# Performance work log

Measured on AMD Instinct MI355X. Metric: run time of the kernel, lower is better.

## Reference

```python
import jax, jax.numpy as jnp
import numpy as np

N_NODES = 100000
N_EDGES = 1600000
EMBED = 64
HEADS = 8
HEAD_DIM = EMBED // HEADS
FFN = 4 * EMBED
EPS = 1e-5


def _layer_norm(x, g, b):
    m = jnp.mean(x, axis=-1, keepdims=True)
    v = jnp.mean(jnp.square(x - m), axis=-1, keepdims=True)
    return (x - m) * jax.lax.rsqrt(v + EPS) * g + b


def setup_inputs() -> dict:
    key = jax.random.key(0)
    ks = jax.random.split(key, 10)
    s = lambda fan_in: 1.0 / np.sqrt(fan_in)
    x = jax.random.normal(ks[0], (N_NODES, EMBED), dtype=jnp.float32)
    edge_indices = jax.random.randint(ks[1], (2, N_EDGES), 0, N_NODES, dtype=jnp.int64)
    attn_w = jax.random.uniform(ks[2], (EMBED, 3 * EMBED), jnp.float32, -s(EMBED), s(EMBED))
    attn_b = jnp.zeros((3 * EMBED,), jnp.float32)
    w1 = jax.random.uniform(ks[3], (EMBED, FFN), jnp.float32, -s(EMBED), s(EMBED))
    b1 = jnp.zeros((FFN,), jnp.float32)
    w2 = jax.random.uniform(ks[4], (FFN, EMBED), jnp.float32, -s(FFN), s(FFN))
    b2 = jnp.zeros((EMBED,), jnp.float32)
    ln1_g = jnp.ones((EMBED,), jnp.float32)
    ln1_b = jnp.zeros((EMBED,), jnp.float32)
    ln2_g = jnp.ones((EMBED,), jnp.float32)
    ln2_b = jnp.zeros((EMBED,), jnp.float32)
    return {"x": x, "edge_indices": edge_indices, "attn_w": attn_w, "attn_b": attn_b,
            "w1": w1, "b1": b1, "w2": w2, "b2": b2,
            "ln1_g": ln1_g, "ln1_b": ln1_b, "ln2_g": ln2_g, "ln2_b": ln2_b}


def _self_attention(x, edge_indices, attn_w, attn_b):
    n = x.shape[0]
    row, col = edge_indices[0], edge_indices[1]
    scale = EMBED ** (-0.5)  # note: original scales by embed_dim**-0.5
    qkv = (x @ attn_w + attn_b).reshape(n, HEADS, 3 * HEAD_DIM)
    q, k, v = jnp.split(qkv, 3, axis=2)  # each [N, H, Dh]
    alpha = jnp.sum(q[row] * k[col], axis=2) * scale  # [E, H]
    # sparse per-row softmax via segment reductions
    m = jax.ops.segment_max(alpha, row, num_segments=n)  # [N, H]
    e = jnp.exp(alpha - m[row])
    denom = jax.ops.segment_sum(e, row, num_segments=n)  # [N, H]
    weights = e / denom[row]  # [E, H]
    vals = v[col] * weights[:, :, None]  # [E, H, Dh]
    out = jax.ops.segment_sum(vals, row, num_segments=n)  # [N, H, Dh]
    return out.reshape(n, EMBED)


def reference(x, edge_indices, attn_w, attn_b, w1, b1, w2, b2, ln1_g, ln1_b, ln2_g, ln2_b):
    # post-norm (norm_first=False), dropout=0
    x = _layer_norm(x + _self_attention(x, edge_indices, attn_w, attn_b), ln1_g, ln1_b)
    ffn = jax.nn.relu(x @ w1 + b1) @ w2 + b2
    x = _layer_norm(x + ffn, ln2_g, ln2_b)
    return x
```

## Files before the change

### kernel.cpp

```cpp
#include <hip/hip_runtime.h>
#include <hip/hip_bf16.h>
#include <hip/hip_fp8.h>


#define WAVE 64
constexpr int BUCKET_SHIFT = 7;
constexpr int NBMAX = 800;

typedef __attribute__((ext_vector_type(8))) short bf16x8;
typedef __attribute__((ext_vector_type(4))) float f32x4;
typedef __attribute__((ext_vector_type(2))) float f32x2;

__device__ __forceinline__ float bfbits_lo(unsigned u) {
  return __uint_as_float(u << 16);
}
__device__ __forceinline__ float bfbits_hi(unsigned u) {
  return __uint_as_float(u & 0xffff0000u);
}
__device__ __forceinline__ unsigned f2bf_pk(float a, float b) {
  unsigned ua = __float_as_uint(a);
  unsigned ub = __float_as_uint(b);
  ua = (ua + 0x7fff + ((ua >> 16) & 1)) >> 16;
  ub = (ub + 0x7fff + ((ub >> 16) & 1)) & 0xffff0000u;
  return ua | ub;
}
__device__ __forceinline__ unsigned short f2bf1(float a) {
  unsigned ua = __float_as_uint(a);
  ua = (ua + 0x7fff + ((ua >> 16) & 1)) >> 16;
  return (unsigned short)ua;
}

#if defined(__has_builtin)
#if __has_builtin(__builtin_amdgcn_cvt_pk_f32_fp8) && \
    __has_builtin(__builtin_amdgcn_cvt_pk_fp8_f32)
#define FP8_HW 1
#endif
#endif

#ifdef FP8_HW
#define FP8PK0(w) __builtin_amdgcn_cvt_pk_f32_fp8((int)(w), false)
#define FP8PK1(w) __builtin_amdgcn_cvt_pk_f32_fp8((int)(w), true)
__device__ __forceinline__ unsigned fp8enc4(float a, float b, float c,
                                            float d) {
  int r = __builtin_amdgcn_cvt_pk_fp8_f32(a, b, 0, false);
  r = __builtin_amdgcn_cvt_pk_fp8_f32(c, d, r, true);
  return (unsigned)r;
}
#else
__device__ __forceinline__ f32x2 fp8pk_sw(unsigned w, int sh) {
  __hip_fp8_e4m3 a, b;
  a.__x = (unsigned char)((w >> sh) & 0xff);
  b.__x = (unsigned char)((w >> (sh + 8)) & 0xff);
  f32x2 r;
  r.x = (float)a;
  r.y = (float)b;
  return r;
}
#define FP8PK0(w) fp8pk_sw((w), 0)
#define FP8PK1(w) fp8pk_sw((w), 16)
__device__ __forceinline__ unsigned fp8enc4(float a, float b, float c,
                                            float d) {
  __hip_fp8_e4m3 qa(a), qb(b), qc(c), qd(d);
  return (unsigned)qa.__x | ((unsigned)qb.__x << 8) |
         ((unsigned)qc.__x << 16) | ((unsigned)qd.__x << 24);
}
#endif

__device__ __forceinline__ float dot8_fp8(uint2 w, const float qv[8]) {
  f32x2 a = FP8PK0(w.x), b = FP8PK1(w.x), c = FP8PK0(w.y), d = FP8PK1(w.y);
  return a.x * qv[0] + a.y * qv[1] + b.x * qv[2] + b.y * qv[3] + c.x * qv[4] +
         c.y * qv[5] + d.x * qv[6] + d.y * qv[7];
}
__device__ __forceinline__ void acc8_fp8(uint2 w, float ee, float acc[8]) {
  f32x2 a = FP8PK0(w.x), b = FP8PK1(w.x), c = FP8PK0(w.y), d = FP8PK1(w.y);
  acc[0] += ee * a.x;
  acc[1] += ee * a.y;
  acc[2] += ee * b.x;
  acc[3] += ee * b.y;
  acc[4] += ee * c.x;
  acc[5] += ee * c.y;
  acc[6] += ee * d.x;
  acc[7] += ee * d.y;
}

__global__ __launch_bounds__(256) void cvt_w2(
    const float* __restrict__ aw, const float* __restrict__ w1,
    const float* __restrict__ w2, unsigned short* __restrict__ awT,
    unsigned short* __restrict__ w1T, unsigned short* __restrict__ w2T) {
  int tid = blockIdx.x * 256 + threadIdx.x;
  int stride = gridDim.x * 256;
  for (int i = tid; i < 192 * 64; i += stride) {
    int nn = i >> 6, kk = i & 63;
    awT[i] = f2bf1(aw[kk * 192 + nn]);
  }
  for (int i = tid; i < 256 * 64; i += stride) {
    int nn = i >> 6, kk = i & 63;
    w1T[i] = f2bf1(w1[kk * 256 + nn]);
  }
  for (int i = tid; i < 64 * 256; i += stride) {
    int nn = i >> 8, kk = i & 255;
    w2T[i] = f2bf1(w2[kk * 64 + nn]);
  }
}

__global__ __launch_bounds__(256) void cvt_x(const float* __restrict__ x,
                                             unsigned short* __restrict__ xb,
                                             int total8) {
  int i = blockIdx.x * 256 + threadIdx.x;
  int stride = gridDim.x * 256;
  const float4* xf = (const float4*)x;
  uint4* xo = (uint4*)xb;
  for (; i < total8; i += stride) {
    float4 a = xf[2 * i], b = xf[2 * i + 1];
    uint4 st = make_uint4(f2bf_pk(a.x, a.y), f2bf_pk(a.z, a.w),
                          f2bf_pk(b.x, b.y), f2bf_pk(b.z, b.w));
    xo[i] = st;
  }
}

template <int NCOLS, int K, int MODE>
__global__ __launch_bounds__(256) void mfma_gemm(
    const unsigned short* __restrict__ A, const unsigned short* __restrict__ BT,
    const float* __restrict__ bias, unsigned short* __restrict__ out_q,
    unsigned char* __restrict__ out_kv8, unsigned short* __restrict__ out_h,
    const unsigned short* __restrict__ resid, const float* __restrict__ g,
    const float* __restrict__ beta, float* __restrict__ out_f, int n) {
  constexpr int KP = K + 8;
  constexpr int NT = NCOLS / 16;
  constexpr int NKC = K / 32;
  __shared__ unsigned short sB[NCOLS * KP];

  const int tid = threadIdx.x;
  {
    const uint4* src = (const uint4*)BT;
    for (int idx = tid; idx < NCOLS * K / 8; idx += 256) {
      int nn = idx / (K / 8), kq = idx % (K / 8);
      *(uint4*)&sB[nn * KP + kq * 8] = src[idx];
    }
  }
  __syncthreads();

  const int wid = tid >> 6, lane = tid & 63;
  const int l15 = lane & 15, quad = lane >> 4;
  const int rowbase = blockIdx.x * 128 + wid * 32;

  bf16x8 afrag[2][NKC];
#pragma unroll
  for (int rg = 0; rg < 2; rg++) {
    int row = rowbase + rg * 16 + l15;
    if (row >= n) row = n - 1;
    const bf16x8* ap = (const bf16x8*)(A + (size_t)row * K);
#pragma unroll
    for (int kc = 0; kc < NKC; kc++) afrag[rg][kc] = ap[kc * 4 + quad];
  }

  f32x4 acc[2][NT];
#pragma unroll
  for (int rg = 0; rg < 2; rg++)
#pragma unroll
    for (int t = 0; t < NT; t++) acc[rg][t] = (f32x4){0.f, 0.f, 0.f, 0.f};

#pragma unroll
  for (int t = 0; t < NT; t++) {
#pragma unroll
    for (int kc = 0; kc < NKC; kc++) {
      bf16x8 b = *(const bf16x8*)&sB[(t * 16 + l15) * KP + kc * 32 + quad * 8];
      acc[0][t] = __builtin_amdgcn_mfma_f32_16x16x32_bf16(b, afrag[0][kc],
                                                          acc[0][t], 0, 0, 0);
      acc[1][t] = __builtin_amdgcn_mfma_f32_16x16x32_bf16(b, afrag[1][kc],
                                                          acc[1][t], 0, 0, 0);
    }
  }

  if (MODE == 0) {
#pragma unroll
    for (int rg = 0; rg < 2; rg++) {
      int row = rowbase + rg * 16 + l15;
      if (row >= n) continue;
#pragma unroll
      for (int t = 0; t < NT; t++) {
        int c0 = t * 16 + quad * 4;
        float4 bb = *(const float4*)&bias[c0];
        float v0 = acc[rg][t].x + bb.x, v1 = acc[rg][t].y + bb.y;
        float v2 = acc[rg][t].z + bb.z, v3 = acc[rg][t].w + bb.w;
        int hh = c0 / 24, rem = c0 % 24;
        if (rem < 8) {
          v0 *= 0.125f;
          v1 *= 0.125f;
          v2 *= 0.125f;
          v3 *= 0.125f;
          *(uint2*)(out_q + (size_t)row * 64 + hh * 8 + rem) =
              make_uint2(f2bf_pk(v0, v1), f2bf_pk(v2, v3));
        } else if (rem < 16) {
          *(unsigned*)(out_kv8 + (size_t)row * 128 + hh * 8 + (rem - 8)) =
              fp8enc4(v0, v1, v2, v3);
        } else {
          *(unsigned*)(out_kv8 + (size_t)row * 128 + 64 + hh * 8 + (rem - 16)) =
              fp8enc4(v0, v1, v2, v3);
        }
      }
    }
  } else if (MODE == 1) {
#pragma unroll
    for (int rg = 0; rg < 2; rg++) {
      int row = rowbase + rg * 16 + l15;
      if (row >= n) continue;
#pragma unroll
      for (int t = 0; t < NT; t++) {
        int c0 = t * 16 + quad * 4;
        float4 bb = *(const float4*)&bias[c0];
        float v0 = fmaxf(acc[rg][t].x + bb.x, 0.f);
        float v1 = fmaxf(acc[rg][t].y + bb.y, 0.f);
        float v2 = fmaxf(acc[rg][t].z + bb.z, 0.f);
        float v3 = fmaxf(acc[rg][t].w + bb.w, 0.f);
        *(uint2*)(out_h + (size_t)row * NCOLS + c0) =
            make_uint2(f2bf_pk(v0, v1), f2bf_pk(v2, v3));
      }
    }
  } else {
#pragma unroll
    for (int rg = 0; rg < 2; rg++) {
      int row = rowbase + rg * 16 + l15;
      bool ok = row < n;
      int rowc = ok ? row : n - 1;
      float vals[4][4];
      float ps = 0.f, pq = 0.f;
#pragma unroll
      for (int t = 0; t < 4; t++) {
        int c0 = t * 16 + quad * 4;
        float4 bb = *(const float4*)&bias[c0];
        uint2 rr = *(const uint2*)&resid[(size_t)rowc * 64 + c0];
        vals[t][0] = acc[rg][t].x + bb.x + bfbits_lo(rr.x);
        vals[t][1] = acc[rg][t].y + bb.y + bfbits_hi(rr.x);
        vals[t][2] = acc[rg][t].z + bb.z + bfbits_lo(rr.y);
        vals[t][3] = acc[rg][t].w + bb.w + bfbits_hi(rr.y);
#pragma unroll
        for (int r = 0; r < 4; r++) {
          ps += vals[t][r];
          pq += vals[t][r] * vals[t][r];
        }
      }
      ps += __shfl_xor(ps, 16);
      ps += __shfl_xor(ps, 32);
      pq += __shfl_xor(pq, 16);
      pq += __shfl_xor(pq, 32);
      float mean = ps * (1.f / 64.f);
      float var = pq * (1.f / 64.f) - mean * mean;
      float inv = rsqrtf(var + 1e-5f);
      if (ok) {
#pragma unroll
        for (int t = 0; t < 4; t++) {
          int c0 = t * 16 + quad * 4;
          float4 gg = *(const float4*)&g[c0];
          float4 be = *(const float4*)&beta[c0];
          float4 o = make_float4((vals[t][0] - mean) * inv * gg.x + be.x,
                                 (vals[t][1] - mean) * inv * gg.y + be.y,
                                 (vals[t][2] - mean) * inv * gg.z + be.z,
                                 (vals[t][3] - mean) * inv * gg.w + be.w);
          *(float4*)&out_f[(size_t)row * 64 + c0] = o;
        }
      }
    }
  }
}

__global__ void detect_kernel(const int* __restrict__ e, unsigned* flag) {
  unsigned v = 0;
  for (int i = threadIdx.x; i < 2048; i += 256) v |= (unsigned)e[2 * i + 1];
#pragma unroll
  for (int m = 1; m < WAVE; m <<= 1) v |= (unsigned)__shfl_xor((int)v, m);
  if ((threadIdx.x & 63) == 0 && v) atomicOr(flag, 1u);
}

__device__ __forceinline__ int edge_row(const int* e, int i, bool is64) {
  return is64 ? e[2 * (size_t)i] : e[i];
}
__device__ __forceinline__ int edge_col(const int* e, int i, int E, bool is64) {
  return is64 ? e[2 * ((size_t)E + i)] : e[(size_t)E + i];
}

__global__ __launch_bounds__(256) void partition_count(
    const int* __restrict__ e, int E, const unsigned* __restrict__ flag,
    int* __restrict__ G, int NB, int CH) {
  __shared__ int h[NBMAX];
  bool is64 = (*flag == 0u);
  for (int b = threadIdx.x; b < NB; b += 256) h[b] = 0;
  __syncthreads();
  int c0 = blockIdx.x * CH, c1 = min(E, c0 + CH);
  for (int i = c0 + threadIdx.x; i < c1; i += 256)
    atomicAdd(&h[edge_row(e, i, is64) >> BUCKET_SHIFT], 1);
  __syncthreads();
  for (int b = threadIdx.x; b < NB; b += 256) G[b * 256 + blockIdx.x] = h[b];
}

__global__ __launch_bounds__(1024) void scan_reduce(const int* __restrict__ in,
                                                    int n,
                                                    int* __restrict__ bsum) {
  __shared__ int sdata[16];
  int tid = threadIdx.x;
  int idx = blockIdx.x * 1024 + tid;
  int v = (idx < n) ? in[idx] : 0;
#pragma unroll
  for (int m = 1; m < WAVE; m <<= 1) v += __shfl_xor(v, m);
  if ((tid & 63) == 0) sdata[tid >> 6] = v;
  __syncthreads();
  if (tid < 16) {
    int s = sdata[tid];
#pragma unroll
    for (int m = 1; m < 16; m <<= 1) s += __shfl_xor(s, m);
    if (tid == 0) bsum[blockIdx.x] = s;
  }
}

__global__ __launch_bounds__(256) void scan_top(const int* __restrict__ bsum,
                                                int nb, int* __restrict__ bpre) {
  __shared__ int wsum[4];
  int tid = threadIdx.x;
  int lane = tid & 63, wid = tid >> 6;
  int v = (tid < nb) ? bsum[tid] : 0;
  int incl = v;
#pragma unroll
  for (int m = 1; m < WAVE; m <<= 1) {
    int t = __shfl_up(incl, m);
    if (lane >= m) incl += t;
  }
  if (lane == 63) wsum[wid] = incl;
  __syncthreads();
  int add = 0;
  for (int w = 0; w < wid; w++) add += wsum[w];
  if (tid < nb) bpre[tid] = add + incl - v;
}

__global__ __launch_bounds__(1024) void scan_apply(
    const int* __restrict__ in, int n, const int* __restrict__ bpre,
    int* __restrict__ outscan) {
  __shared__ int wtot[16];
  __shared__ int wexcl[16];
  int tid = threadIdx.x;
  int idx = blockIdx.x * 1024 + tid;
  int v = (idx < n) ? in[idx] : 0;
  int incl = v;
#pragma unroll
  for (int m = 1; m < WAVE; m <<= 1) {
    int t = __shfl_up(incl, m);
    if ((tid & 63) >= m) incl += t;
  }
  int wid = tid >> 6;
  if ((tid & 63) == 63) wtot[wid] = incl;
  __syncthreads();
  if (tid < 16) {
    int w = wtot[tid];
    int wi = w;
#pragma unroll
    for (int m = 1; m < 16; m <<= 1) {
      int t = __shfl_up(wi, m);
      if (tid >= m) wi += t;
    }
    wexcl[tid] = wi - w;
  }
  __syncthreads();
  if (idx < n) outscan[idx] = bpre[blockIdx.x] + wexcl[wid] + incl - v;
}

__global__ __launch_bounds__(256) void partition_scatter(
    const int* __restrict__ e, int E, const unsigned* __restrict__ flag,
    const int* __restrict__ scanG, unsigned* __restrict__ ebuf, int NB,
    int CH) {
  __shared__ int base[NBMAX];
  bool is64 = (*flag == 0u);
  for (int b = threadIdx.x; b < NB; b += 256)
    base[b] = scanG[b * 256 + blockIdx.x];
  __syncthreads();
  int c0 = blockIdx.x * CH, c1 = min(E, c0 + CH);
  for (int i = c0 + threadIdx.x; i < c1; i += 256) {
    int r = edge_row(e, i, is64);
    int c = edge_col(e, i, E, is64);
    int pos = atomicAdd(&base[r >> BUCKET_SHIFT], 1);
    ebuf[pos] = ((unsigned)(r & 127) << 17) | (unsigned)c;
  }
}

__global__ __launch_bounds__(256) void bucket_csr(
    const unsigned* __restrict__ ebuf, const int* __restrict__ scanG,
    int* __restrict__ ecol, int* __restrict__ rowstart, int n, int NB, int E) {
  __shared__ int cnt[128], offs[128], cur[128];
  const int b = blockIdx.x;
  const int tid = threadIdx.x;
  const int start = scanG[b * 256];
  const int end = (b + 1 < NB) ? scanG[(b + 1) * 256] : E;
  if (tid < 128) cnt[tid] = 0;
  __syncthreads();
  for (int i = start + tid; i < end; i += 256)
    atomicAdd(&cnt[(ebuf[i] >> 17) & 127], 1);
  __syncthreads();
  if (tid < 128) offs[tid] = cnt[tid];
  __syncthreads();
  for (int s = 1; s < 128; s <<= 1) {
    int t = 0;
    if (tid < 128 && tid >= s) t = offs[tid - s];
    __syncthreads();
    if (tid < 128) offs[tid] += t;
    __syncthreads();
  }
  if (tid < 128) {
    int excl = offs[tid] - cnt[tid];
    cur[tid] = start + excl;
    int gr = (b << BUCKET_SHIFT) + tid;
    if (gr < n) rowstart[gr] = start + excl;
  }
  if (b == NB - 1 && tid == 0) rowstart[n] = E;
  __syncthreads();
  for (int i = start + tid; i < end; i += 256) {
    unsigned p = ebuf[i];
    int pos = atomicAdd(&cur[(p >> 17) & 127], 1);
    ecol[pos] = (int)(p & 0x1FFFF);
  }
}

__global__ __launch_bounds__(256) void attn_ln_kernel(
    const unsigned short* __restrict__ xb,
    const unsigned short* __restrict__ qbuf,
    const unsigned char* __restrict__ kv8, const int* __restrict__ rowstart,
    const int* __restrict__ ecol, const float* __restrict__ g,
    const float* __restrict__ beta, unsigned short* __restrict__ x1b, int n) {
  int wave = threadIdx.x >> 6;
  int lane = threadIdx.x & 63;
  int node = blockIdx.x * 4 + wave;
  if (node >= n) return;
  const int e = lane >> 3, h = lane & 7;

  uint4 qp = ((const uint4*)(qbuf + (size_t)node * 64))[h];
  float qv[8] = {bfbits_lo(qp.x), bfbits_hi(qp.x), bfbits_lo(qp.y),
                 bfbits_hi(qp.y), bfbits_lo(qp.z), bfbits_hi(qp.z),
                 bfbits_lo(qp.w), bfbits_hi(qp.w)};

  int start = rowstart[node];
  int cnt = rowstart[node + 1] - start;
  float den = 0.f;
  float acc[8] = {0.f, 0.f, 0.f, 0.f, 0.f, 0.f, 0.f, 0.f};

  int iters = (cnt + 7) >> 3;
  int it = 0;
  for (; it + 2 <= iters; it += 2) {
    int i0 = it * 8 + e;
    int i1 = i0 + 8;
    bool v1 = i1 < cnt;
    int c0 = ecol[start + i0];
    int c1 = ecol[start + (v1 ? i1 : i0)];
    const unsigned char* r0 = kv8 + (size_t)c0 * 128 + h * 8;
    const unsigned char* r1 = kv8 + (size_t)c1 * 128 + h * 8;
    uint2 kw0 = *(const uint2*)r0;
    uint2 vw0 = *(const uint2*)(r0 + 64);
    uint2 kw1 = *(const uint2*)r1;
    uint2 vw1 = *(const uint2*)(r1 + 64);
    float a0 = dot8_fp8(kw0, qv);
    float a1 = dot8_fp8(kw1, qv);
    float e0 = __expf(a0);
    float e1 = v1 ? __expf(a1) : 0.f;
    den += e0 + e1;
    acc8_fp8(vw0, e0, acc);
    acc8_fp8(vw1, e1, acc);
  }
  if (it < iters) {
    int i0 = it * 8 + e;
    bool v0 = i0 < cnt;
    int c0 = ecol[start + (v0 ? i0 : 0)];
    const unsigned char* r0 = kv8 + (size_t)c0 * 128 + h * 8;
    uint2 kw0 = *(const uint2*)r0;
    uint2 vw0 = *(const uint2*)(r0 + 64);
    float a0 = dot8_fp8(kw0, qv);
    float e0 = v0 ? __expf(a0) : 0.f;
    den += e0;
    acc8_fp8(vw0, e0, acc);
  }

#pragma unroll
  for (int m = 8; m < 64; m <<= 1) {
    den += __shfl_xor(den, m);
#pragma unroll
    for (int j = 0; j < 8; j++) acc[j] += __shfl_xor(acc[j], m);
  }

  float invden = (cnt > 0) ? 1.f / den : 0.f;

  uint4 xr = *(const uint4*)(xb + (size_t)node * 64 + h * 8);
  float v[8];
  v[0] = bfbits_lo(xr.x) + acc[0] * invden;
  v[1] = bfbits_hi(xr.x) + acc[1] * invden;
  v[2] = bfbits_lo(xr.y) + acc[2] * invden;
  v[3] = bfbits_hi(xr.y) + acc[3] * invden;
  v[4] = bfbits_lo(xr.z) + acc[4] * invden;
  v[5] = bfbits_hi(xr.z) + acc[5] * invden;
  v[6] = bfbits_lo(xr.w) + acc[6] * invden;
  v[7] = bfbits_hi(xr.w) + acc[7] * invden;

  float ps = 0.f;
#pragma unroll
  for (int j = 0; j < 8; j++) ps += v[j];
#pragma unroll
  for (int m = 1; m < 8; m <<= 1) ps += __shfl_xor(ps, m);
  float mean = ps * (1.f / 64.f);
  float pq = 0.f;
#pragma unroll
  for (int j = 0; j < 8; j++) {
    float d = v[j] - mean;
    pq += d * d;
  }
#pragma unroll
  for (int m = 1; m < 8; m <<= 1) pq += __shfl_xor(pq, m);
  float inv = rsqrtf(pq * (1.f / 64.f) + 1e-5f);

  if (e == 0) {
    const float4* gr = (const float4*)(g + h * 8);
    const float4* br = (const float4*)(beta + h * 8);
    float4 ga = gr[0], gb = gr[1];
    float4 ba = br[0], bb = br[1];
    float o[8];
    o[0] = (v[0] - mean) * inv * ga.x + ba.x;
    o[1] = (v[1] - mean) * inv * ga.y + ba.y;
    o[2] = (v[2] - mean) * inv * ga.z + ba.z;
    o[3] = (v[3] - mean) * inv * ga.w + ba.w;
    o[4] = (v[4] - mean) * inv * gb.x + bb.x;
    o[5] = (v[5] - mean) * inv * gb.y + bb.y;
    o[6] = (v[6] - mean) * inv * gb.z + bb.z;
    o[7] = (v[7] - mean) * inv * gb.w + bb.w;
    *(uint4*)(x1b + (size_t)node * 64 + h * 8) =
        make_uint4(f2bf_pk(o[0], o[1]), f2bf_pk(o[2], o[3]),
                   f2bf_pk(o[4], o[5]), f2bf_pk(o[6], o[7]));
  }
}

extern "C" void kernel_launch(void* const* d_in, const int* in_sizes, int n_in,
                              void* d_out, int out_size, void* d_ws,
                              size_t ws_size, hipStream_t stream) {
  const float* x = (const float*)d_in[0];
  const int* edges = (const int*)d_in[1];
  const float* attn_w = (const float*)d_in[2];
  const float* attn_b = (const float*)d_in[3];
  const float* w1 = (const float*)d_in[4];
  const float* b1 = (const float*)d_in[5];
  const float* w2 = (const float*)d_in[6];
  const float* b2 = (const float*)d_in[7];
  const float* g1 = (const float*)d_in[8];
  const float* bb1 = (const float*)d_in[9];
  const float* g2 = (const float*)d_in[10];
  const float* bb2 = (const float*)d_in[11];

  const int N = in_sizes[0] / 64;
  const int E = in_sizes[1] / 2;
  const int NB = (N + 127) >> BUCKET_SHIFT;
  const int CH = (E + 255) / 256;
  const int NG = NB * 256;

  char* ws = (char*)d_ws;
  size_t oq = 0;
  size_t okv = oq + (size_t)N * 128;
  size_t ox1b = okv + (size_t)N * 128;
  size_t oxb = ox1b + (size_t)N * 128;
  size_t oh = oxb + (size_t)N * 128;
  size_t oawT = oh + (size_t)N * 512;
  size_t ow1T = oawT + 192 * 64 * 2;
  size_t ow2T = ow1T + 256 * 64 * 2;
  size_t oG = ow2T + 64 * 256 * 2;
  size_t oscanG = oG + (size_t)NG * 4;
  size_t oebuf = oscanG + (size_t)NG * 4;
  size_t oecol = oebuf + (size_t)E * 4;
  size_t orowstart = oecol + (size_t)E * 4;
  size_t obsum = orowstart + (size_t)(N + 4) * 4;
  size_t obpre = obsum + 1024;
  size_t oflag = obpre + 1024;

  unsigned short* qbuf = (unsigned short*)(ws + oq);
  unsigned char* kv8 = (unsigned char*)(ws + okv);
  unsigned short* x1b = (unsigned short*)(ws + ox1b);
  unsigned short* xb = (unsigned short*)(ws + oxb);
  unsigned short* hbuf = (unsigned short*)(ws + oh);
  unsigned short* awT = (unsigned short*)(ws + oawT);
  unsigned short* w1T = (unsigned short*)(ws + ow1T);
  unsigned short* w2T = (unsigned short*)(ws + ow2T);
  int* G = (int*)(ws + oG);
  int* scanG = (int*)(ws + oscanG);
  unsigned* ebuf = (unsigned*)(ws + oebuf);
  int* ecol = (int*)(ws + oecol);
  int* rowstart = (int*)(ws + orowstart);
  int* bsum = (int*)(ws + obsum);
  int* bpre = (int*)(ws + obpre);
  unsigned* flag = (unsigned*)(ws + oflag);

  hipMemsetAsync(flag, 0, 4, stream);

  cvt_w2<<<32, 256, 0, stream>>>(attn_w, w1, w2, awT, w1T, w2T);
  cvt_x<<<512, 256, 0, stream>>>(x, xb, N * 8);

  detect_kernel<<<1, 256, 0, stream>>>(edges, flag);
  partition_count<<<256, 256, 0, stream>>>(edges, E, flag, G, NB, CH);
  int nscan = (NG + 1023) / 1024;
  scan_reduce<<<nscan, 1024, 0, stream>>>(G, NG, bsum);
  scan_top<<<1, 256, 0, stream>>>(bsum, nscan, bpre);
  scan_apply<<<nscan, 1024, 0, stream>>>(G, NG, bpre, scanG);
  partition_scatter<<<256, 256, 0, stream>>>(edges, E, flag, scanG, ebuf, NB,
                                             CH);
  bucket_csr<<<NB, 256, 0, stream>>>(ebuf, scanG, ecol, rowstart, N, NB, E);

  const int gblocks = (N + 127) / 128;

  mfma_gemm<192, 64, 0><<<gblocks, 256, 0, stream>>>(
      xb, awT, attn_b, qbuf, kv8, nullptr, nullptr, nullptr, nullptr, nullptr,
      N);

  attn_ln_kernel<<<(N + 3) / 4, 256, 0, stream>>>(xb, qbuf, kv8, rowstart,
                                                  ecol, g1, bb1, x1b, N);

  mfma_gemm<256, 64, 1><<<gblocks, 256, 0, stream>>>(
      x1b, w1T, b1, nullptr, nullptr, hbuf, nullptr, nullptr, nullptr, nullptr,
      N);

  mfma_gemm<64, 256, 2><<<gblocks, 256, 0, stream>>>(
      hbuf, w2T, b2, nullptr, nullptr, nullptr, x1b, g2, bb2, (float*)d_out,
      N);
}
```

Before: 281.2 us.

## Fuse x conversion into GEMM and simplify edge bucketing pipeline

```diff
diff --git a/kernel.cpp b/kernel.cpp
--- a/kernel.cpp
+++ b/kernel.cpp
@@ -10,6 +10,11 @@
 typedef __attribute__((ext_vector_type(8))) short bf16x8;
 typedef __attribute__((ext_vector_type(4))) float f32x4;
 typedef __attribute__((ext_vector_type(2))) float f32x2;
+
+union BF8 {
+  bf16x8 v;
+  unsigned u[4];
+};
 
 __device__ __forceinline__ float bfbits_lo(unsigned u) {
   return __uint_as_float(u << 16);
@@ -83,6 +88,25 @@
   acc[7] += ee * d.y;
 }
 
+__device__ __forceinline__ bool detect_is64_block(const int* __restrict__ e,
+                                                  int* sflag) {
+  if (threadIdx.x == 0) *sflag = 0;
+  __syncthreads();
+  unsigned v = 0;
+  for (int i = threadIdx.x; i < 2048; i += blockDim.x)
+    v |= (unsigned)e[2 * i + 1];
+  if (v) atomicOr(sflag, 1);
+  __syncthreads();
+  return *sflag == 0;
+}
+
+__device__ __forceinline__ int edge_row(const int* e, int i, bool is64) {
+  return is64 ? e[2 * (size_t)i] : e[i];
+}
+__device__ __forceinline__ int edge_col(const int* e, int i, int E, bool is64) {
+  return is64 ? e[2 * ((size_t)E + i)] : e[(size_t)E + i];
+}
+
 __global__ __launch_bounds__(256) void cvt_w2(
     const float* __restrict__ aw, const float* __restrict__ w1,
     const float* __restrict__ w2, unsigned short* __restrict__ awT,
@@ -103,24 +127,124 @@
   }
 }
 
-__global__ __launch_bounds__(256) void cvt_x(const float* __restrict__ x,
-                                             unsigned short* __restrict__ xb,
-                                             int total8) {
-  int i = blockIdx.x * 256 + threadIdx.x;
-  int stride = gridDim.x * 256;
-  const float4* xf = (const float4*)x;
-  uint4* xo = (uint4*)xb;
-  for (; i < total8; i += stride) {
-    float4 a = xf[2 * i], b = xf[2 * i + 1];
-    uint4 st = make_uint4(f2bf_pk(a.x, a.y), f2bf_pk(a.z, a.w),
-                          f2bf_pk(b.x, b.y), f2bf_pk(b.z, b.w));
-    xo[i] = st;
-  }
-}
-
-template <int NCOLS, int K, int MODE>
+__global__ __launch_bounds__(256) void bucket_count(const int* __restrict__ e,
+                                                    int E,
+                                                    int* __restrict__ tot,
+                                                    int NB, int CH) {
+  __shared__ int h[NBMAX];
+  __shared__ int sflag;
+  bool is64 = detect_is64_block(e, &sflag);
+  for (int b = threadIdx.x; b < NB; b += 256) h[b] = 0;
+  __syncthreads();
+  int c0 = blockIdx.x * CH, c1 = min(E, c0 + CH);
+  for (int i = c0 + threadIdx.x; i < c1; i += 256)
+    atomicAdd(&h[edge_row(e, i, is64) >> BUCKET_SHIFT], 1);
+  __syncthreads();
+  for (int b = threadIdx.x; b < NB; b += 256)
+    if (h[b]) atomicAdd(&tot[b], h[b]);
+}
+
+__global__ __launch_bounds__(1024) void scan_buckets(
+    const int* __restrict__ tot, int NB, int* __restrict__ bucketstart,
+    int* __restrict__ cursor) {
+  __shared__ int wtot[16], wexcl[16];
+  int tid = threadIdx.x;
+  int lane = tid & 63, wid = tid >> 6;
+  int v = (tid < NB) ? tot[tid] : 0;
+  int incl = v;
+#pragma unroll
+  for (int m = 1; m < WAVE; m <<= 1) {
+    int t = __shfl_up(incl, m);
+    if (lane >= m) incl += t;
+  }
+  if (lane == 63) wtot[wid] = incl;
+  __syncthreads();
+  if (tid < 16) {
+    int w = wtot[tid];
+    int wi = w;
+#pragma unroll
+    for (int m = 1; m < 16; m <<= 1) {
+      int t = __shfl_up(wi, m);
+      if (tid >= m) wi += t;
+    }
+    wexcl[tid] = wi - w;
+  }
+  __syncthreads();
+  int excl = wexcl[wid] + incl - v;
+  if (tid < NB) {
+    bucketstart[tid] = excl;
+    cursor[tid] = excl;
+  }
+  if (tid == NB - 1) bucketstart[NB] = excl + v;
+}
+
+__global__ __launch_bounds__(256) void bucket_place(const int* __restrict__ e,
+                                                    int E,
+                                                    int* __restrict__ cursor,
+                                                    unsigned* __restrict__ ebuf,
+                                                    int NB, int CH) {
+  __shared__ int cnt[NBMAX];
+  __shared__ int sflag;
+  bool is64 = detect_is64_block(e, &sflag);
+  for (int b = threadIdx.x; b < NB; b += 256) cnt[b] = 0;
+  __syncthreads();
+  int c0 = blockIdx.x * CH, c1 = min(E, c0 + CH);
+  for (int i = c0 + threadIdx.x; i < c1; i += 256)
+    atomicAdd(&cnt[edge_row(e, i, is64) >> BUCKET_SHIFT], 1);
+  __syncthreads();
+  for (int b = threadIdx.x; b < NB; b += 256) {
+    int c = cnt[b];
+    cnt[b] = c ? atomicAdd(&cursor[b], c) : 0;
+  }
+  __syncthreads();
+  for (int i = c0 + threadIdx.x; i < c1; i += 256) {
+    int r = edge_row(e, i, is64);
+    int c = edge_col(e, i, E, is64);
+    int pos = atomicAdd(&cnt[r >> BUCKET_SHIFT], 1);
+    ebuf[pos] = ((unsigned)(r & 127) << 17) | (unsigned)c;
+  }
+}
+
+__global__ __launch_bounds__(256) void bucket_csr(
+    const unsigned* __restrict__ ebuf, const int* __restrict__ bucketstart,
+    int* __restrict__ ecol, int* __restrict__ rowstart, int n, int NB, int E) {
+  __shared__ int cnt[128], offs[128], cur[128];
+  const int b = blockIdx.x;
+  const int tid = threadIdx.x;
+  const int start = bucketstart[b];
+  const int end = bucketstart[b + 1];
+  if (tid < 128) cnt[tid] = 0;
+  __syncthreads();
+  for (int i = start + tid; i < end; i += 256)
+    atomicAdd(&cnt[(ebuf[i] >> 17) & 127], 1);
+  __syncthreads();
+  if (tid < 128) offs[tid] = cnt[tid];
+  __syncthreads();
+  for (int s = 1; s < 128; s <<= 1) {
+    int t = 0;
+    if (tid < 128 && tid >= s) t = offs[tid - s];
+    __syncthreads();
+    if (tid < 128) offs[tid] += t;
+    __syncthreads();
+  }
+  if (tid < 128) {
+    int excl = offs[tid] - cnt[tid];
+    cur[tid] = start + excl;
+    int gr = (b << BUCKET_SHIFT) + tid;
+    if (gr < n) rowstart[gr] = start + excl;
+  }
+  if (b == NB - 1 && tid == 0) rowstart[n] = E;
+  __syncthreads();
+  for (int i = start + tid; i < end; i += 256) {
+    unsigned p = ebuf[i];
+    int pos = atomicAdd(&cur[(p >> 17) & 127], 1);
+    ecol[pos] = (int)(p & 0x1FFFF);
+  }
+}
+
+template <int NCOLS, int K, int MODE, bool AFP32>
 __global__ __launch_bounds__(256) void mfma_gemm(
-    const unsigned short* __restrict__ A, const unsigned short* __restrict__ BT,
+    const void* __restrict__ A, const unsigned short* __restrict__ BT,
     const float* __restrict__ bias, unsigned short* __restrict__ out_q,
     unsigned char* __restrict__ out_kv8, unsigned short* __restrict__ out_h,
     const unsigned short* __restrict__ resid, const float* __restrict__ g,
@@ -149,9 +273,24 @@
   for (int rg = 0; rg < 2; rg++) {
     int row = rowbase + rg * 16 + l15;
     if (row >= n) row = n - 1;
-    const bf16x8* ap = (const bf16x8*)(A + (size_t)row * K);
-#pragma unroll
-    for (int kc = 0; kc < NKC; kc++) afrag[rg][kc] = ap[kc * 4 + quad];
+    if (AFP32) {
+      const float* Af = ((const float*)A) + (size_t)row * K;
+#pragma unroll
+      for (int kc = 0; kc < NKC; kc++) {
+        float4 u0 = *(const float4*)(Af + kc * 32 + quad * 8);
+        float4 u1 = *(const float4*)(Af + kc * 32 + quad * 8 + 4);
+        BF8 t;
+        t.u[0] = f2bf_pk(u0.x, u0.y);
+        t.u[1] = f2bf_pk(u0.z, u0.w);
+        t.u[2] = f2bf_pk(u1.x, u1.y);
+        t.u[3] = f2bf_pk(u1.z, u1.w);
+        afrag[rg][kc] = t.v;
+      }
+    } else {
+      const bf16x8* ap = (const bf16x8*)((const unsigned short*)A + (size_t)row * K);
+#pragma unroll
+      for (int kc = 0; kc < NKC; kc++) afrag[rg][kc] = ap[kc * 4 + quad];
+    }
   }
 
   f32x4 acc[2][NT];
@@ -264,162 +403,8 @@
   }
 }
 
-__global__ void detect_kernel(const int* __restrict__ e, unsigned* flag) {
-  unsigned v = 0;
-  for (int i = threadIdx.x; i < 2048; i += 256) v |= (unsigned)e[2 * i + 1];
-#pragma unroll
-  for (int m = 1; m < WAVE; m <<= 1) v |= (unsigned)__shfl_xor((int)v, m);
-  if ((threadIdx.x & 63) == 0 && v) atomicOr(flag, 1u);
-}
-
-__device__ __forceinline__ int edge_row(const int* e, int i, bool is64) {
-  return is64 ? e[2 * (size_t)i] : e[i];
-}
-__device__ __forceinline__ int edge_col(const int* e, int i, int E, bool is64) {
-  return is64 ? e[2 * ((size_t)E + i)] : e[(size_t)E + i];
-}
-
-__global__ __launch_bounds__(256) void partition_count(
-    const int* __restrict__ e, int E, const unsigned* __restrict__ flag,
-    int* __restrict__ G, int NB, int CH) {
-  __shared__ int h[NBMAX];
-  bool is64 = (*flag == 0u);
-  for (int b = threadIdx.x; b < NB; b += 256) h[b] = 0;
-  __syncthreads();
-  int c0 = blockIdx.x * CH, c1 = min(E, c0 + CH);
-  for (int i = c0 + threadIdx.x; i < c1; i += 256)
-    atomicAdd(&h[edge_row(e, i, is64) >> BUCKET_SHIFT], 1);
-  __syncthreads();
-  for (int b = threadIdx.x; b < NB; b += 256) G[b * 256 + blockIdx.x] = h[b];
-}
-
-__global__ __launch_bounds__(1024) void scan_reduce(const int* __restrict__ in,
-                                                    int n,
-                                                    int* __restrict__ bsum) {
-  __shared__ int sdata[16];
-  int tid = threadIdx.x;
-  int idx = blockIdx.x * 1024 + tid;
-  int v = (idx < n) ? in[idx] : 0;
-#pragma unroll
-  for (int m = 1; m < WAVE; m <<= 1) v += __shfl_xor(v, m);
-  if ((tid & 63) == 0) sdata[tid >> 6] = v;
-  __syncthreads();
-  if (tid < 16) {
-    int s = sdata[tid];
-#pragma unroll
-    for (int m = 1; m < 16; m <<= 1) s += __shfl_xor(s, m);
-    if (tid == 0) bsum[blockIdx.x] = s;
-  }
-}
-
-__global__ __launch_bounds__(256) void scan_top(const int* __restrict__ bsum,
-                                                int nb, int* __restrict__ bpre) {
-  __shared__ int wsum[4];
-  int tid = threadIdx.x;
-  int lane = tid & 63, wid = tid >> 6;
-  int v = (tid < nb) ? bsum[tid] : 0;
-  int incl = v;
-#pragma unroll
-  for (int m = 1; m < WAVE; m <<= 1) {
-    int t = __shfl_up(incl, m);
-    if (lane >= m) incl += t;
-  }
-  if (lane == 63) wsum[wid] = incl;
-  __syncthreads();
-  int add = 0;
-  for (int w = 0; w < wid; w++) add += wsum[w];
-  if (tid < nb) bpre[tid] = add + incl - v;
-}
-
-__global__ __launch_bounds__(1024) void scan_apply(
-    const int* __restrict__ in, int n, const int* __restrict__ bpre,
-    int* __restrict__ outscan) {
-  __shared__ int wtot[16];
-  __shared__ int wexcl[16];
-  int tid = threadIdx.x;
-  int idx = blockIdx.x * 1024 + tid;
-  int v = (idx < n) ? in[idx] : 0;
-  int incl = v;
-#pragma unroll
-  for (int m = 1; m < WAVE; m <<= 1) {
-    int t = __shfl_up(incl, m);
-    if ((tid & 63) >= m) incl += t;
-  }
-  int wid = tid >> 6;
-  if ((tid & 63) == 63) wtot[wid] = incl;
-  __syncthreads();
-  if (tid < 16) {
-    int w = wtot[tid];
-    int wi = w;
-#pragma unroll
-    for (int m = 1; m < 16; m <<= 1) {
-      int t = __shfl_up(wi, m);
-      if (tid >= m) wi += t;
-    }
-    wexcl[tid] = wi - w;
-  }
-  __syncthreads();
-  if (idx < n) outscan[idx] = bpre[blockIdx.x] + wexcl[wid] + incl - v;
-}
-
-__global__ __launch_bounds__(256) void partition_scatter(
-    const int* __restrict__ e, int E, const unsigned* __restrict__ flag,
-    const int* __restrict__ scanG, unsigned* __restrict__ ebuf, int NB,
-    int CH) {
-  __shared__ int base[NBMAX];
-  bool is64 = (*flag == 0u);
-  for (int b = threadIdx.x; b < NB; b += 256)
-    base[b] = scanG[b * 256 + blockIdx.x];
-  __syncthreads();
-  int c0 = blockIdx.x * CH, c1 = min(E, c0 + CH);
-  for (int i = c0 + threadIdx.x; i < c1; i += 256) {
-    int r = edge_row(e, i, is64);
-    int c = edge_col(e, i, E, is64);
-    int pos = atomicAdd(&base[r >> BUCKET_SHIFT], 1);
-    ebuf[pos] = ((unsigned)(r & 127) << 17) | (unsigned)c;
-  }
-}
-
-__global__ __launch_bounds__(256) void bucket_csr(
-    const unsigned* __restrict__ ebuf, const int* __restrict__ scanG,
-    int* __restrict__ ecol, int* __restrict__ rowstart, int n, int NB, int E) {
-  __shared__ int cnt[128], offs[128], cur[128];
-  const int b = blockIdx.x;
-  const int tid = threadIdx.x;
-  const int start = scanG[b * 256];
-  const int end = (b + 1 < NB) ? scanG[(b + 1) * 256] : E;
-  if (tid < 128) cnt[tid] = 0;
-  __syncthreads();
-  for (int i = start + tid; i < end; i += 256)
-    atomicAdd(&cnt[(ebuf[i] >> 17) & 127], 1);
-  __syncthreads();
-  if (tid < 128) offs[tid] = cnt[tid];
-  __syncthreads();
-  for (int s = 1; s < 128; s <<= 1) {
-    int t = 0;
-    if (tid < 128 && tid >= s) t = offs[tid - s];
-    __syncthreads();
-    if (tid < 128) offs[tid] += t;
-    __syncthreads();
-  }
-  if (tid < 128) {
-    int excl = offs[tid] - cnt[tid];
-    cur[tid] = start + excl;
-    int gr = (b << BUCKET_SHIFT) + tid;
-    if (gr < n) rowstart[gr] = start + excl;
-  }
-  if (b == NB - 1 && tid == 0) rowstart[n] = E;
-  __syncthreads();
-  for (int i = start + tid; i < end; i += 256) {
-    unsigned p = ebuf[i];
-    int pos = atomicAdd(&cur[(p >> 17) & 127], 1);
-    ecol[pos] = (int)(p & 0x1FFFF);
-  }
-}
-
 __global__ __launch_bounds__(256) void attn_ln_kernel(
-    const unsigned short* __restrict__ xb,
-    const unsigned short* __restrict__ qbuf,
+    const float* __restrict__ x, const unsigned short* __restrict__ qbuf,
     const unsigned char* __restrict__ kv8, const int* __restrict__ rowstart,
     const int* __restrict__ ecol, const float* __restrict__ g,
     const float* __restrict__ beta, unsigned short* __restrict__ x1b, int n) {
@@ -483,16 +468,17 @@
 
   float invden = (cnt > 0) ? 1.f / den : 0.f;
 
-  uint4 xr = *(const uint4*)(xb + (size_t)node * 64 + h * 8);
+  const float4* xr = (const float4*)(x + (size_t)node * 64 + h * 8);
+  float4 xa = xr[0], xb4 = xr[1];
   float v[8];
-  v[0] = bfbits_lo(xr.x) + acc[0] * invden;
-  v[1] = bfbits_hi(xr.x) + acc[1] * invden;
-  v[2] = bfbits_lo(xr.y) + acc[2] * invden;
-  v[3] = bfbits_hi(xr.y) + acc[3] * invden;
-  v[4] = bfbits_lo(xr.z) + acc[4] * invden;
-  v[5] = bfbits_hi(xr.z) + acc[5] * invden;
-  v[6] = bfbits_lo(xr.w) + acc[6] * invden;
-  v[7] = bfbits_hi(xr.w) + acc[7] * invden;
+  v[0] = xa.x + acc[0] * invden;
+  v[1] = xa.y + acc[1] * invden;
+  v[2] = xa.z + acc[2] * invden;
+  v[3] = xa.w + acc[3] * invden;
+  v[4] = xb4.x + acc[4] * invden;
+  v[5] = xb4.y + acc[5] * invden;
+  v[6] = xb4.z + acc[6] * invden;
+  v[7] = xb4.w + acc[7] * invden;
 
   float ps = 0.f;
 #pragma unroll
@@ -550,72 +536,60 @@
   const int E = in_sizes[1] / 2;
   const int NB = (N + 127) >> BUCKET_SHIFT;
   const int CH = (E + 255) / 256;
-  const int NG = NB * 256;
 
   char* ws = (char*)d_ws;
   size_t oq = 0;
   size_t okv = oq + (size_t)N * 128;
   size_t ox1b = okv + (size_t)N * 128;
-  size_t oxb = ox1b + (size_t)N * 128;
-  size_t oh = oxb + (size_t)N * 128;
+  size_t oh = ox1b + (size_t)N * 128;
   size_t oawT = oh + (size_t)N * 512;
   size_t ow1T = oawT + 192 * 64 * 2;
   size_t ow2T = ow1T + 256 * 64 * 2;
-  size_t oG = ow2T + 64 * 256 * 2;
-  size_t oscanG = oG + (size_t)NG * 4;
-  size_t oebuf = oscanG + (size_t)NG * 4;
+  size_t oebuf = ow2T + 64 * 256 * 2;
   size_t oecol = oebuf + (size_t)E * 4;
   size_t orowstart = oecol + (size_t)E * 4;
-  size_t obsum = orowstart + (size_t)(N + 4) * 4;
-  size_t obpre = obsum + 1024;
-  size_t oflag = obpre + 1024;
+  size_t otot = orowstart + (size_t)(N + 4) * 4;
+  size_t obstart = otot + (size_t)(NBMAX) * 4;
+  size_t ocursor = obstart + (size_t)(NBMAX + 4) * 4;
 
   unsigned short* qbuf = (unsigned short*)(ws + oq);
   unsigned char* kv8 = (unsigned char*)(ws + okv);
   unsigned short* x1b = (unsigned short*)(ws + ox1b);
-  unsigned short* xb = (unsigned short*)(ws + oxb);
   unsigned short* hbuf = (unsigned short*)(ws + oh);
   unsigned short* awT = (unsigned short*)(ws + oawT);
   unsigned short* w1T = (unsigned short*)(ws + ow1T);
   unsigned short* w2T = (unsigned short*)(ws + ow2T);
-  int* G = (int*)(ws + oG);
-  int* scanG = (int*)(ws + oscanG);
   unsigned* ebuf = (unsigned*)(ws + oebuf);
   int* ecol = (int*)(ws + oecol);
   int* rowstart = (int*)(ws + orowstart);
-  int* bsum = (int*)(ws + obsum);
-  int* bpre = (int*)(ws + obpre);
-  unsigned* flag = (unsigned*)(ws + oflag);
-
-  hipMemsetAsync(flag, 0, 4, stream);
+  int* tot = (int*)(ws + otot);
+  int* bucketstart = (int*)(ws + obstart);
+  int* cursor = (int*)(ws + ocursor);
+
+  hipMemsetAsync(tot, 0, (size_t)NB * 4, stream);
 
   cvt_w2<<<32, 256, 0, stream>>>(attn_w, w1, w2, awT, w1T, w2T);
-  cvt_x<<<512, 256, 0, stream>>>(x, xb, N * 8);
-
-  detect_kernel<<<1, 256, 0, stream>>>(edges, flag);
-  partition_count<<<256, 256, 0, stream>>>(edges, E, flag, G, NB, CH);
-  int nscan = (NG + 1023) / 1024;
-  scan_reduce<<<nscan, 1024, 0, stream>>>(G, NG, bsum);
-  scan_top<<<1, 256, 0, stream>>>(bsum, nscan, bpre);
-  scan_apply<<<nscan, 1024, 0, stream>>>(G, NG, bpre, scanG);
-  partition_scatter<<<256, 256, 0, stream>>>(edges, E, flag, scanG, ebuf, NB,
-                                             CH);
-  bucket_csr<<<NB, 256, 0, stream>>>(ebuf, scanG, ecol, rowstart, N, NB, E);
+
+  bucket_count<<<256, 256, 0, stream>>>(edges, E, tot, NB, CH);
+  scan_buckets<<<1, 1024, 0, stream>>>(tot, NB, bucketstart, cursor);
+  bucket_place<<<256, 256, 0, stream>>>(edges, E, cursor, ebuf, NB, CH);
+  bucket_csr<<<NB, 256, 0, stream>>>(ebuf, bucketstart, ecol, rowstart, N, NB,
+                                     E);
 
   const int gblocks = (N + 127) / 128;
 
-  mfma_gemm<192, 64, 0><<<gblocks, 256, 0, stream>>>(
-      xb, awT, attn_b, qbuf, kv8, nullptr, nullptr, nullptr, nullptr, nullptr,
+  mfma_gemm<192, 64, 0, true><<<gblocks, 256, 0, stream>>>(
+      x, awT, attn_b, qbuf, kv8, nullptr, nullptr, nullptr, nullptr, nullptr,
       N);
 
-  attn_ln_kernel<<<(N + 3) / 4, 256, 0, stream>>>(xb, qbuf, kv8, rowstart,
-                                                  ecol, g1, bb1, x1b, N);
-
-  mfma_gemm<256, 64, 1><<<gblocks, 256, 0, stream>>>(
+  attn_ln_kernel<<<(N + 3) / 4, 256, 0, stream>>>(x, qbuf, kv8, rowstart, ecol,
+                                                  g1, bb1, x1b, N);
+
+  mfma_gemm<256, 64, 1, false><<<gblocks, 256, 0, stream>>>(
       x1b, w1T, b1, nullptr, nullptr, hbuf, nullptr, nullptr, nullptr, nullptr,
       N);
 
-  mfma_gemm<64, 256, 2><<<gblocks, 256, 0, stream>>>(
+  mfma_gemm<64, 256, 2, false><<<gblocks, 256, 0, stream>>>(
       hbuf, w2T, b2, nullptr, nullptr, nullptr, x1b, g2, bb2, (float*)d_out,
       N);
 }
```

New measurement: 284.0 us. No clear change (+1.0%).
